# Kernel optimization log

Hardware: AMD Instinct MI355X
Metric: run time of the kernel (lower is better)

The kernel has to match this reference:

```python
import jax, jax.numpy as jnp
import numpy as np

K = 5            # self.k
MARGIN_CB = 0.05  # neighborhood_ranking_crossbrain default margin
MARGIN_NRC = 0.4  # self.margin used in partial_nrc_loss
MAX_PAIRS = 6
EPS = 1e-8


def _norm(x):
    return x / jnp.sqrt(jnp.sum(x * x, axis=-1, keepdims=True) + 1e-12)


def _cos_dist_pair(a, b):
    s = jnp.clip(jnp.sum(a * b, axis=-1), -1.0 + EPS, 1.0 - EPS)
    return 1.0 - s


def _pairwise_cos_dist(x, y):
    return 1.0 - _norm(x) @ _norm(y).T


def _sq_dist(x):
    # squared euclidean distance -- same argsort order as torch.cdist
    sq = jnp.sum(x * x, axis=-1)
    return jnp.maximum(sq[:, None] + sq[None, :] - 2.0 * (x @ x.T), 0.0)


def _crossbrain(z1, z2, key):
    # neighborhood_ranking_crossbrain with match_idx = identity (as in forward)
    N = z1.shape[0]
    D1 = jax.lax.stop_gradient(_sq_dist(z1))      # ranking only, no grad
    neigh = jnp.argsort(D1, axis=-1)[:, 1:K + 1]  # (N, K) nearest neighbors
    # sample K distinct negatives per token excluding {n} U neigh[n]:
    scores = jax.random.uniform(key, (N, N))
    rows = jnp.arange(N)
    scores = scores.at[rows[:, None], neigh].set(-jnp.inf)
    scores = scores.at[rows, rows].set(-jnp.inf)
    _, neg = jax.lax.top_k(scores, K)             # (N, K)
    z2n = _norm(z2)
    anchor = z2n[:, None, :]                      # (N,1,C)
    d_pos = _cos_dist_pair(anchor, z2n[neigh])    # (N, K)
    d_neg = _cos_dist_pair(anchor, z2n[neg])      # (N, K)
    return jnp.mean(jax.nn.relu(d_pos - d_neg + MARGIN_CB))


def _nrc_partial(A, B, key):
    # partial_matches_mnn + nrc_on_partial, fully vectorized & masked
    T = A.shape[0]
    D = jax.lax.stop_gradient(_pairwise_cos_dist(A, B))
    b_of_a = jnp.argmin(D, axis=1)
    a_of_b = jnp.argmin(D, axis=0)
    ar = jnp.arange(T)
    mutual = ar == a_of_b[b_of_a]                 # matched A tokens (injective)
    idxB_of_A = jnp.where(mutual, b_of_a, -1)
    is_matched_B = (jnp.zeros(T, jnp.int32).at[b_of_a].add(mutual.astype(jnp.int32)) > 0)
    DA = jax.lax.stop_gradient(_pairwise_cos_dist(A, A))
    neigh = jnp.argsort(DA, axis=-1)[:, 1:K + 1]  # (T, K)
    DB = _pairwise_cos_dist(B, B)                 # grads flow through DB
    posB = idxB_of_A[neigh]                       # (T, K)
    pos_mask = posB >= 0
    # negative pool: unmatched B tokens (stable argsort puts False first)
    order = jnp.argsort(is_matched_B)
    neg_count = jnp.maximum(T - jnp.sum(is_matched_B.astype(jnp.int32)), 1)
    r = jax.random.randint(key, (T, K), 0, T)
    negB = order[r % neg_count]                   # sample with replacement
    uB = jnp.maximum(idxB_of_A, 0)[:, None]
    d_pos = DB[uB, jnp.maximum(posB, 0)]
    d_neg = DB[uB, negB]
    hinge = jax.nn.relu(d_pos - d_neg + MARGIN_NRC) * pos_mask
    per_tok = jnp.sum(hinge, axis=1) / jnp.maximum(jnp.sum(pos_mask, axis=1), 1)
    valid = mutual & jnp.any(pos_mask, axis=1)
    cnt = jnp.sum(valid.astype(jnp.float32))
    return jnp.where(cnt > 0, jnp.sum(per_tok * valid) / jnp.maximum(cnt, 1.0), 0.0)


def _partial_nrc_loss(z1, z2, key, seed):
    Bn = z1.shape[0]
    pairs = [(p, q) for p in range(Bn) for q in range(Bn) if p != q]
    rng = np.random.RandomState(seed)
    if len(pairs) > MAX_PAIRS:
        sel = rng.permutation(len(pairs))[:MAX_PAIRS]
        pairs = [pairs[i] for i in sel]
    ps = jnp.array([p for p, _ in pairs])
    qs = jnp.array([q for _, q in pairs])
    keys = jax.random.split(key, len(pairs))
    losses = jax.vmap(_nrc_partial)(z1[ps], z2[qs], keys)
    return jnp.mean(losses)


def _taco_loss(z1, z2):
    Bn = z1.shape[0]
    base = jax.random.key(42)
    k1, k2, k3, k4 = jax.random.split(base, 4)
    loss2 = (jnp.sum(jax.vmap(_crossbrain)(z1, z2, jax.random.split(k1, Bn)))
             + jnp.sum(jax.vmap(_crossbrain)(z2, z1, jax.random.split(k2, Bn)))) / Bn
    loss3 = _partial_nrc_loss(z1, z2, k3, 0) + _partial_nrc_loss(z2, z1, k4, 1)
    return 10.0 * loss2 + 10.0 * loss3


def setup_inputs() -> dict:
    key = jax.random.key(0)
    k1, k2 = jax.random.split(key)
    Bn, T, C = 4, 2048, 768
    z1 = jax.random.normal(k1, (Bn, T, C), dtype=jnp.float32)
    z2 = jax.random.normal(k2, (Bn, T, C), dtype=jnp.float32)
    return {"z1": z1, "z2": z2}


def reference(z1, z2):
    return _taco_loss(z1, z2)
```

## Files before the change

kernel.cpp:

```cpp
#include <hip/hip_runtime.h>
#include <cstdint>
#include <cstddef>

#define TT 2048
#define CC 768
#define KK 5
#define PCAP 64

typedef __attribute__((ext_vector_type(8))) short short8;
typedef __attribute__((ext_vector_type(4))) short short4v;
typedef __attribute__((ext_vector_type(4))) float float4v;

struct PairTab { int sa[12]; int sb[12]; };
struct PairMap { int src[12]; int tr[12]; };

#define N_SELF_BLK (8 * 136)
#define TP 132

__device__ __forceinline__ unsigned int mix_hash(unsigned int a, unsigned int b) {
  unsigned long long x = (((unsigned long long)a) << 32) | (unsigned long long)b;
  x ^= x >> 33; x *= 0xff51afd7ed558ccdULL;
  x ^= x >> 33; x *= 0xc4ceb9fe1a85ec53ULL;
  x ^= x >> 33;
  return (unsigned int)(x & 0xffffffffu);
}

__device__ __forceinline__ unsigned short f2bf(float x) {
  union { float f; unsigned int u; } v; v.f = x;
  unsigned int r = v.u + 0x7fffu + ((v.u >> 16) & 1u);
  return (unsigned short)(r >> 16);
}

__device__ __forceinline__ float bf2f(unsigned short u) {
  union { unsigned int i; float f; } v; v.i = ((unsigned int)u) << 16; return v.f;
}

__device__ __forceinline__ void gload_lds16(const void* g, void* l) {
  __builtin_amdgcn_global_load_lds(
      (const __attribute__((address_space(1))) unsigned int*)g,
      (__attribute__((address_space(3))) unsigned int*)l, 16, 0, 0);
}

__device__ __forceinline__ bool lexlt(float k1, int i1, float k2, int i2) {
  return k1 < k2 || (k1 == k2 && i1 < i2);
}

#define INS5(kk_, ii_, L)                                                        \
  if (lexlt(kk_, ii_, L##k[4], L##i[4])) {                                       \
    L##k[4] = kk_; L##i[4] = ii_;                                                \
    if (lexlt(L##k[4], L##i[4], L##k[3], L##i[3])) {                             \
      float tk = L##k[3]; int ti_ = L##i[3]; L##k[3] = L##k[4]; L##i[3] = L##i[4]; L##k[4] = tk; L##i[4] = ti_; \
      if (lexlt(L##k[3], L##i[3], L##k[2], L##i[2])) {                           \
        tk = L##k[2]; ti_ = L##i[2]; L##k[2] = L##k[3]; L##i[2] = L##i[3]; L##k[3] = tk; L##i[3] = ti_; \
        if (lexlt(L##k[2], L##i[2], L##k[1], L##i[1])) {                         \
          tk = L##k[1]; ti_ = L##i[1]; L##k[1] = L##k[2]; L##i[1] = L##i[2]; L##k[2] = tk; L##i[2] = ti_; \
          if (lexlt(L##k[1], L##i[1], L##k[0], L##i[0])) {                       \
            tk = L##k[0]; ti_ = L##i[0]; L##k[0] = L##k[1]; L##i[0] = L##i[1]; L##k[1] = tk; L##i[1] = ti_; \
          }                                                                      \
        }                                                                        \
      }                                                                          \
    }                                                                            \
  }

__global__ __launch_bounds__(192) void prep_kernel(const float* __restrict__ z1, const float* __restrict__ z2,
                                                   unsigned short* __restrict__ zb, float* __restrict__ sq,
                                                   float* __restrict__ inv) {
  int r = blockIdx.x;
  const float* p = (r < 4 * TT) ? (z1 + (size_t)r * CC) : (z2 + (size_t)(r - 4 * TT) * CC);
  unsigned short* o = zb + (size_t)r * CC;
  float4 v = ((const float4*)p)[threadIdx.x];
  float s = v.x * v.x + v.y * v.y + v.z * v.z + v.w * v.w;
  ushort4 u;
  u.x = f2bf(v.x); u.y = f2bf(v.y); u.z = f2bf(v.z); u.w = f2bf(v.w);
  ((ushort4*)o)[threadIdx.x] = u;
#pragma unroll
  for (int off = 32; off > 0; off >>= 1) s += __shfl_down(s, off, 64);
  __shared__ float wred[3];
  int lane = threadIdx.x & 63, w = threadIdx.x >> 6;
  if (lane == 0) wred[w] = s;
  __syncthreads();
  if (threadIdx.x == 0) {
    float tot = wred[0] + wred[1] + wred[2];
    sq[r] = tot; inv[r] = rsqrtf(tot + 1e-12f);
  }
}

struct SmemKL { unsigned short As[128 * 64]; unsigned short Bs[128 * 64]; };
union SmemU {
  SmemKL st;
  unsigned short tile[128 * TP];
};

__device__ __forceinline__ void gram_mainloop(const unsigned short* __restrict__ A,
                                              const unsigned short* __restrict__ B,
                                              int bm, int bn, SmemKL& st, float4v (&acc)[4][4]) {
  const int lane = threadIdx.x & 63, waveId = threadIdx.x >> 6;
  const int wm = (waveId >> 1) * 64, wn = (waveId & 1) * 64;
  const int lrow = lane & 15, lquad = lane >> 4;
  for (int kk = 0; kk < CC; kk += 64) {
#pragma unroll
    for (int c = 0; c < 4; ++c) {
      int l = c * 256 + threadIdx.x;
      int row = l >> 3, pc = l & 7;
      int sc = pc ^ (row & 7);
      gload_lds16(A + (size_t)(bm + row) * CC + kk + sc * 8, &st.As[l * 8]);
      gload_lds16(B + (size_t)(bn + row) * CC + kk + sc * 8, &st.Bs[l * 8]);
    }
    __syncthreads();
#pragma unroll
    for (int h = 0; h < 2; ++h) {
      short8 af[4], bfr[4];
#pragma unroll
      for (int i = 0; i < 4; ++i) {
        int ra = wm + i * 16 + lrow;
        int ca = (h * 4 + lquad) ^ (ra & 7);
        af[i] = *(const short8*)&st.As[ra * 64 + ca * 8];
        int rb = wn + i * 16 + lrow;
        int cb2 = (h * 4 + lquad) ^ (rb & 7);
        bfr[i] = *(const short8*)&st.Bs[rb * 64 + cb2 * 8];
      }
#pragma unroll
      for (int i = 0; i < 4; ++i)
#pragma unroll
        for (int j = 0; j < 4; ++j)
          acc[i][j] = __builtin_amdgcn_mfma_f32_16x16x32_bf16(af[i], bfr[j], acc[i][j], 0, 0, 0);
    }
    __syncthreads();
  }
}

__global__ __launch_bounds__(256, 4) void gram_self(const unsigned short* __restrict__ zb,
                                                    unsigned short* __restrict__ gram) {
  __shared__ SmemU sm;
  const int bid = blockIdx.x;
  int s = bid / 136;
  int t = bid % 136;
  int ti = 0;
  while (t >= 16 - ti) { t -= 16 - ti; ++ti; }
  int tj = ti + t;
  int bm = ti * 128, bn = tj * 128;
  const unsigned short* A = zb + (size_t)s * TT * CC;

  float4v acc[4][4];
#pragma unroll
  for (int i = 0; i < 4; ++i)
#pragma unroll
    for (int j = 0; j < 4; ++j) acc[i][j] = (float4v){0.f, 0.f, 0.f, 0.f};

  gram_mainloop(A, A, bm, bn, sm.st, acc);

  const int lane = threadIdx.x & 63, waveId = threadIdx.x >> 6;
  const int wm = (waveId >> 1) * 64, wn = (waveId & 1) * 64;
  const int lrow = lane & 15, lquad = lane >> 4;

#pragma unroll
  for (int i = 0; i < 4; ++i)
#pragma unroll
    for (int j = 0; j < 4; ++j)
#pragma unroll
      for (int r = 0; r < 4; ++r) {
        int lr = wm + i * 16 + lquad * 4 + r;
        int lc = wn + j * 16 + lrow;
        sm.tile[lr * TP + lc] = f2bf(acc[i][j][r]);
      }
  __syncthreads();
  unsigned short* G = gram + (size_t)s * TT * TT;
  for (int it = 0; it < 16; ++it) {
    int task = it * 256 + threadIdx.x;
    int r = task >> 5;
    int c = task & 31;
    short4v v = *(const short4v*)&sm.tile[r * TP + c * 4];
    *(short4v*)&G[(size_t)(bm + r) * TT + bn + c * 4] = v;
  }
  if (bm != bn) {
    for (int it = 0; it < 16; ++it) {
      int task = it * 256 + threadIdx.x;
      int cc = task >> 5;
      int q = task & 31;
      short4v v;
      v[0] = (short)sm.tile[(q * 4 + 0) * TP + cc];
      v[1] = (short)sm.tile[(q * 4 + 1) * TP + cc];
      v[2] = (short)sm.tile[(q * 4 + 2) * TP + cc];
      v[3] = (short)sm.tile[(q * 4 + 3) * TP + cc];
      *(short4v*)&G[(size_t)(bn + cc) * TT + bm + q * 4] = v;
    }
  }
}

__global__ __launch_bounds__(256, 4) void gram_cross(const unsigned short* __restrict__ zb,
                                                     const float* __restrict__ invAll, PairTab tab,
                                                     float* __restrict__ prow_v, int* __restrict__ prow_i,
                                                     float* __restrict__ pcol_v, int* __restrict__ pcol_i) {
  __shared__ SmemKL smk;
  __shared__ float sInvA[128], sInvB[128];
  __shared__ float rowv[2][128]; __shared__ int rowi[2][128];
  __shared__ float colv[2][128]; __shared__ int coli[2][128];

  const int cbid = blockIdx.x;
  const int p = cbid >> 8;
  const int tile = cbid & 255;
  const int bn = (tile & 15) * 128;
  const int bm = (tile >> 4) * 128;
  const unsigned short* A = zb + (size_t)tab.sa[p] * TT * CC;
  const unsigned short* B = zb + (size_t)tab.sb[p] * TT * CC;
  if (threadIdx.x < 128) sInvA[threadIdx.x] = invAll[(size_t)tab.sa[p] * TT + bm + threadIdx.x];
  else sInvB[threadIdx.x - 128] = invAll[(size_t)tab.sb[p] * TT + bn + threadIdx.x - 128];

  float4v acc[4][4];
#pragma unroll
  for (int i = 0; i < 4; ++i)
#pragma unroll
    for (int j = 0; j < 4; ++j) acc[i][j] = (float4v){0.f, 0.f, 0.f, 0.f};

  gram_mainloop(A, B, bm, bn, smk, acc);

  const int lane = threadIdx.x & 63, waveId = threadIdx.x >> 6;
  const int wm = (waveId >> 1) * 64, wn = (waveId & 1) * 64;
  const int lrow = lane & 15, lquad = lane >> 4;

  float rbv[4][4]; int rbi[4][4];
#pragma unroll
  for (int i = 0; i < 4; ++i)
#pragma unroll
    for (int r = 0; r < 4; ++r) { rbv[i][r] = INFINITY; rbi[i][r] = TT; }
#pragma unroll
  for (int i = 0; i < 4; ++i)
#pragma unroll
    for (int j = 0; j < 4; ++j) {
      int col = bn + wn + j * 16 + lrow;
      float ivb = sInvB[wn + j * 16 + lrow];
#pragma unroll
      for (int r = 0; r < 4; ++r) {
        float v = -acc[i][j][r] * ivb;
        if (v < rbv[i][r]) { rbv[i][r] = v; rbi[i][r] = col; }
      }
    }
#pragma unroll
  for (int m = 1; m <= 8; m <<= 1) {
#pragma unroll
    for (int i = 0; i < 4; ++i)
#pragma unroll
      for (int r = 0; r < 4; ++r) {
        float v2 = __shfl_xor(rbv[i][r], m, 64);
        int i2 = __shfl_xor(rbi[i][r], m, 64);
        if (v2 < rbv[i][r] || (v2 == rbv[i][r] && i2 < rbi[i][r])) { rbv[i][r] = v2; rbi[i][r] = i2; }
      }
  }
  if (lrow == 0) {
#pragma unroll
    for (int i = 0; i < 4; ++i)
#pragma unroll
      for (int r = 0; r < 4; ++r) {
        int lr = wm + i * 16 + lquad * 4 + r;
        rowv[wn >> 6][lr] = rbv[i][r]; rowi[wn >> 6][lr] = rbi[i][r];
      }
  }

  float cbv[4]; int cbi[4];
#pragma unroll
  for (int j = 0; j < 4; ++j) { cbv[j] = INFINITY; cbi[j] = TT; }
#pragma unroll
  for (int j = 0; j < 4; ++j)
#pragma unroll
    for (int i = 0; i < 4; ++i)
#pragma unroll
      for (int r = 0; r < 4; ++r) {
        int lr = wm + i * 16 + lquad * 4 + r;
        float v = -acc[i][j][r] * sInvA[lr];
        if (v < cbv[j]) { cbv[j] = v; cbi[j] = bm + lr; }
      }
#pragma unroll
  for (int m = 16; m <= 32; m <<= 1) {
#pragma unroll
    for (int j = 0; j < 4; ++j) {
      float v2 = __shfl_xor(cbv[j], m, 64);
      int i2 = __shfl_xor(cbi[j], m, 64);
      if (v2 < cbv[j] || (v2 == cbv[j] && i2 < cbi[j])) { cbv[j] = v2; cbi[j] = i2; }
    }
  }
  if (lquad == 0) {
#pragma unroll
    for (int j = 0; j < 4; ++j) {
      int lc = wn + j * 16 + lrow;
      colv[wm >> 6][lc] = cbv[j]; coli[wm >> 6][lc] = cbi[j];
    }
  }
  __syncthreads();

  int bj = bn >> 7, bi2 = bm >> 7;
  if (threadIdx.x < 128) {
    int t = threadIdx.x;
    float v0 = rowv[0][t], v1 = rowv[1][t];
    int i0 = rowi[0][t], i1 = rowi[1][t];
    bool take1 = (v1 < v0) || (v1 == v0 && i1 < i0);
    prow_v[((size_t)p * 16 + bj) * TT + bm + t] = take1 ? v1 : v0;
    prow_i[((size_t)p * 16 + bj) * TT + bm + t] = take1 ? i1 : i0;
  } else {
    int t = threadIdx.x - 128;
    float v0 = colv[0][t], v1 = colv[1][t];
    int i0 = coli[0][t], i1 = coli[1][t];
    bool take1 = (v1 < v0) || (v1 == v0 && i1 < i0);
    pcol_v[((size_t)p * 16 + bi2) * TT + bn + t] = take1 ? v1 : v0;
    pcol_i[((size_t)p * 16 + bi2) * TT + bn + t] = take1 ? i1 : i0;
  }
}

__device__ void top5_row_full(const unsigned short* __restrict__ G, const float* __restrict__ sq,
                              const float* __restrict__ inv, int i, int lane,
                              int* __restrict__ o0, int* __restrict__ o1) {
  float ak[5]; int ai[5];
  float bk[5]; int bi[5];
#pragma unroll
  for (int t = 0; t < 5; ++t) { ak[t] = INFINITY; ai[t] = TT; bk[t] = INFINITY; bi[t] = TT; }
#pragma unroll
  for (int step = 0; step < 8; ++step) {
    int j4 = (step * 64 + lane) * 4;
    ushort4 g4u = *(const ushort4*)&G[j4];
    float4 s4 = *(const float4*)&sq[j4];
    float4 v4 = *(const float4*)&inv[j4];
#pragma unroll
    for (int c = 0; c < 4; ++c) {
      int j = j4 + c;
      float g = bf2f((c == 0) ? g4u.x : (c == 1) ? g4u.y : (c == 2) ? g4u.z : g4u.w);
      float sv = (c == 0) ? s4.x : (c == 1) ? s4.y : (c == 2) ? s4.z : s4.w;
      float iv = (c == 0) ? v4.x : (c == 1) ? v4.y : (c == 2) ? v4.z : v4.w;
      float k0 = (j == i) ? INFINITY : sv - 2.f * g;
      float k1 = (j == i) ? INFINITY : -g * iv;
      INS5(k0, j, a)
      INS5(k1, j, b)
    }
  }
#pragma unroll
  for (int m = 1; m <= 32; m <<= 1) {
    float ok[5]; int oi[5];
#pragma unroll
    for (int t = 0; t < 5; ++t) { ok[t] = __shfl_xor(ak[t], m, 64); oi[t] = __shfl_xor(ai[t], m, 64); }
#pragma unroll
    for (int t = 0; t < 5; ++t) { INS5(ok[t], oi[t], a) }
#pragma unroll
    for (int t = 0; t < 5; ++t) { ok[t] = __shfl_xor(bk[t], m, 64); oi[t] = __shfl_xor(bi[t], m, 64); }
#pragma unroll
    for (int t = 0; t < 5; ++t) { INS5(ok[t], oi[t], b) }
  }
  if (lane < KK) {
    int v0 = (lane == 0) ? ai[0] : (lane == 1) ? ai[1] : (lane == 2) ? ai[2] : (lane == 3) ? ai[3] : ai[4];
    int v1 = (lane == 0) ? bi[0] : (lane == 1) ? bi[1] : (lane == 2) ? bi[2] : (lane == 3) ? bi[3] : bi[4];
    o0[lane] = v0;
    o1[lane] = v1;
  }
}

__device__ void top5_body(int s, int bx, const unsigned short* __restrict__ gram,
                          const float* __restrict__ sqAll, const float* __restrict__ invAll,
                          int* __restrict__ out0, int* __restrict__ out1) {
  int w = threadIdx.x >> 6, lane = threadIdx.x & 63;
  int i = bx * 4 + w;
  const unsigned short* G = gram + (size_t)s * TT * TT + (size_t)i * TT;
  const float* sq = sqAll + (size_t)s * TT;
  const float* inv = invAll + (size_t)s * TT;

  __shared__ ushort4 rowc4[4][TT / 4];
  __shared__ float pvv[4][2][PCAP];
  __shared__ int pix[4][2][PCAP];
  __shared__ int pcnt[4][2];
  if (lane < 2) pcnt[w][lane] = 0;

  float mn0 = INFINITY, mn1 = INFINITY;
#pragma unroll
  for (int step = 0; step < 8; ++step) {
    int jc = step * 64 + lane;
    int j4 = jc * 4;
    ushort4 g4u = *(const ushort4*)&G[j4];
    rowc4[w][jc] = g4u;
    float4 s4 = *(const float4*)&sq[j4];
    float4 v4 = *(const float4*)&inv[j4];
#pragma unroll
    for (int c = 0; c < 4; ++c) {
      int j = j4 + c;
      float g = bf2f((c == 0) ? g4u.x : (c == 1) ? g4u.y : (c == 2) ? g4u.z : g4u.w);
      float sv = (c == 0) ? s4.x : (c == 1) ? s4.y : (c == 2) ? s4.z : s4.w;
      float iv = (c == 0) ? v4.x : (c == 1) ? v4.y : (c == 2) ? v4.z : v4.w;
      float k0 = (j == i) ? INFINITY : sv - 2.f * g;
      float k1 = (j == i) ? INFINITY : -g * iv;
      mn0 = fminf(mn0, k0);
      mn1 = fminf(mn1, k1);
    }
  }
#pragma unroll
  for (int m = 1; m <= 4; m <<= 1) {
    mn0 = fminf(mn0, __shfl_xor(mn0, m, 64));
    mn1 = fminf(mn1, __shfl_xor(mn1, m, 64));
  }
  float gv0[8], gv1[8];
#pragma unroll
  for (int g = 0; g < 8; ++g) {
    gv0[g] = __shfl(mn0, g * 8, 64);
    gv1[g] = __shfl(mn1, g * 8, 64);
  }
  float T0 = 0.f, T1 = 0.f;
#pragma unroll
  for (int g = 0; g < 8; ++g) {
    int r0 = 0, r1 = 0;
#pragma unroll
    for (int h = 0; h < 8; ++h) {
      r0 += ((gv0[h] < gv0[g]) || (gv0[h] == gv0[g] && h < g)) ? 1 : 0;
      r1 += ((gv1[h] < gv1[g]) || (gv1[h] == gv1[g] && h < g)) ? 1 : 0;
    }
    if (r0 == 4) T0 = gv0[g];
    if (r1 == 4) T1 = gv1[g];
  }

#pragma unroll
  for (int step = 0; step < 8; ++step) {
    int jc = step * 64 + lane;
    int j4 = jc * 4;
    ushort4 g4u = rowc4[w][jc];
    float4 s4 = *(const float4*)&sq[j4];
    float4 v4 = *(const float4*)&inv[j4];
#pragma unroll
    for (int c = 0; c < 4; ++c) {
      int j = j4 + c;
      float g = bf2f((c == 0) ? g4u.x : (c == 1) ? g4u.y : (c == 2) ? g4u.z : g4u.w);
      float sv = (c == 0) ? s4.x : (c == 1) ? s4.y : (c == 2) ? s4.z : s4.w;
      float iv = (c == 0) ? v4.x : (c == 1) ? v4.y : (c == 2) ? v4.z : v4.w;
      float k0 = (j == i) ? INFINITY : sv - 2.f * g;
      float k1 = (j == i) ? INFINITY : -g * iv;
      bool c0 = (k0 <= T0), c1 = (k1 <= T1);
      if (__any(c0)) {
        if (c0) {
          int q = atomicAdd(&pcnt[w][0], 1);
          if (q < PCAP) { pvv[w][0][q] = k0; pix[w][0][q] = j; }
        }
      }
      if (__any(c1)) {
        if (c1) {
          int q = atomicAdd(&pcnt[w][1], 1);
          if (q < PCAP) { pvv[w][1][q] = k1; pix[w][1][q] = j; }
        }
      }
    }
  }

  int c0n = pcnt[w][0], c1n = pcnt[w][1];
  if (c0n > PCAP || c1n > PCAP) {
    top5_row_full(G, sq, inv, i, lane,
                  out0 + ((size_t)s * TT + i) * KK, out1 + ((size_t)s * TT + i) * KK);
    return;
  }
  {
    float cv = (lane < c0n) ? pvv[w][0][lane] : INFINITY;
    int ci = (lane < c0n) ? pix[w][0][lane] : TT;
    int r = 0;
    for (int t = 0; t < c0n; ++t) {
      float ov = pvv[w][0][t]; int oi = pix[w][0][t];
      r += lexlt(ov, oi, cv, ci) ? 1 : 0;
    }
    if (lane < c0n && r < KK) out0[((size_t)s * TT + i) * KK + r] = ci;
  }
  {
    float cv = (lane < c1n) ? pvv[w][1][lane] : INFINITY;
    int ci = (lane < c1n) ? pix[w][1][lane] : TT;
    int r = 0;
    for (int t = 0; t < c1n; ++t) {
      float ov = pvv[w][1][t]; int oi = pix[w][1][t];
      r += lexlt(ov, oi, cv, ci) ? 1 : 0;
    }
    if (lane < c1n && r < KK) out1[((size_t)s * TT + i) * KK + r] = ci;
  }
}

__device__ void argmin_body(int bx, int p, const float* __restrict__ prow_v, const int* __restrict__ prow_i,
                            const float* __restrict__ pcol_v, const int* __restrict__ pcol_i,
                            const PairMap& pm,
                            int* __restrict__ b_of_a, int* __restrict__ a_of_b) {
  int u = pm.src[p];
  bool tr = pm.tr[p] != 0;
  int t = bx * 256 + threadIdx.x;
  int isRow = t < TT;
  int x = isRow ? t : t - TT;
  bool useRow = (isRow != 0) != tr;
  const float* pv = (useRow ? prow_v : pcol_v) + (size_t)u * 16 * TT;
  const int* pi = (useRow ? prow_i : pcol_i) + (size_t)u * 16 * TT;
  float best = INFINITY; int bidx = TT;
  for (int s = 0; s < 16; ++s) {
    float v = pv[(size_t)s * TT + x]; int id = pi[(size_t)s * TT + x];
    if (v < best || (v == best && id < bidx)) { best = v; bidx = id; }
  }
  if (isRow) b_of_a[(size_t)p * TT + x] = bidx;
  else       a_of_b[(size_t)p * TT + x] = bidx;
}

__global__ __launch_bounds__(256) void top5_argmin_fused(const unsigned short* __restrict__ gram,
                                                         const float* __restrict__ sqAll,
                                                         const float* __restrict__ invAll,
                                                         int* __restrict__ out0, int* __restrict__ out1,
                                                         const float* __restrict__ prow_v, const int* __restrict__ prow_i,
                                                         const float* __restrict__ pcol_v, const int* __restrict__ pcol_i,
                                                         PairMap pm,
                                                         int* __restrict__ b_of_a, int* __restrict__ a_of_b) {
  unsigned int b = blockIdx.x;
  if (b < 4096) {
    top5_body((int)(b >> 9), (int)(b & 511), gram, sqAll, invAll, out0, out1);
  } else {
    unsigned int t = b - 4096;
    argmin_body((int)(t & 15), (int)(t >> 4), prow_v, prow_i, pcol_v, pcol_i, pm, b_of_a, a_of_b);
  }
}

__device__ void cb_hinge_body(int bx, int c, const unsigned short* __restrict__ gram, const float* __restrict__ invAll,
                              const int* __restrict__ neigh1, float* __restrict__ cb_acc) {
  int i0 = bx * 64;
  int sa = c, sb = (c < 4) ? (c + 4) : (c - 4);
  const unsigned short* Gs = gram + (size_t)sb * TT * TT;
  const float* invB = invAll + (size_t)sb * TT;
  const int* neighA = neigh1 + (size_t)sa * TT * KK;
  unsigned int seed = 0x13579BDFu + 0x9E3779B9u * (unsigned)c;
  int tid = threadIdx.x;

  __shared__ int targ[64][10];
  __shared__ float sval[64][10];
  for (int t = tid; t < 64 * KK; t += 256) targ[t / KK][t % KK] = neighA[(size_t)i0 * KK + t];
  __syncthreads();
  if (tid < 64) {
    int i = i0 + tid;
    int pos[KK];
#pragma unroll
    for (int k = 0; k < KK; ++k) pos[k] = targ[tid][k];
    unsigned int ctr = 0;
    for (int k = 0; k < KK; ++k) {
      int cand;
      while (true) {
        unsigned int h = mix_hash(seed ^ (unsigned)i, ctr++);
        cand = (int)(h & (TT - 1));
        bool bad = (cand == i);
        for (int t = 0; t < KK; ++t) bad = bad || (cand == pos[t]);
        for (int t = 0; t < k; ++t) bad = bad || (cand == targ[tid][KK + t]);
        if (!bad) break;
      }
      targ[tid][KK + k] = cand;
    }
  }
  __syncthreads();
  for (int t = tid; t < 640; t += 256) {
    int il = t / 10, k = t % 10;
    int tt = targ[il][k];
    sval[il][k] = bf2f(Gs[(size_t)(i0 + il) * TT + tt]) * invB[tt];
  }
  __syncthreads();
  if (tid < 64) {
    int i = i0 + tid;
    float ii = invB[i];
    const float lo = -1.f + 1e-8f, hi = 1.f - 1e-8f;
    float hsum = 0.f;
#pragma unroll
    for (int k = 0; k < KK; ++k) {
      float sp = fminf(fmaxf(sval[tid][k] * ii, lo), hi);
      float sn = fminf(fmaxf(sval[tid][KK + k] * ii, lo), hi);
      float h = sn - sp + 0.05f;
      hsum += (h > 0.f) ? h : 0.f;
    }
#pragma unroll
    for (int off = 32; off > 0; off >>= 1) hsum += __shfl_down(hsum, off, 64);
    if (tid == 0) atomicAdd(&cb_acc[c], hsum);
  }
}

__device__ void mutual_body(int p, const int* __restrict__ b_of_a_all,
                            const int* __restrict__ a_of_b_all,
                            int* __restrict__ idxB_all, int* __restrict__ matchedB_all,
                            int* __restrict__ unmatched_all, int* __restrict__ scalars_all) {
  const int* b_of_a = b_of_a_all + (size_t)p * TT;
  const int* a_of_b = a_of_b_all + (size_t)p * TT;
  int* idxB_of_A = idxB_all + (size_t)p * TT;
  int* matchedB = matchedB_all + (size_t)p * TT;
  int* unmatched = unmatched_all + (size_t)p * TT;
  __shared__ int cnt_sh;
  for (int j = threadIdx.x; j < TT; j += 256) matchedB[j] = 0;
  __syncthreads();
  for (int i = threadIdx.x; i < TT; i += 256) {
    int b = b_of_a[i];
    bool mut = (a_of_b[b] == i);
    idxB_of_A[i] = mut ? b : -1;
    if (mut) matchedB[b] = 1;
  }
  __syncthreads();
  if (threadIdx.x == 0) cnt_sh = 0;
  __syncthreads();
  for (int j = threadIdx.x; j < TT; j += 256) {
    if (!matchedB[j]) { int q = atomicAdd(&cnt_sh, 1); unmatched[q] = j; }
  }
  __syncthreads();
  if (threadIdx.x == 0) {
    int c = cnt_sh;
    if (c == 0) { unmatched[0] = 0; c = 1; }
    scalars_all[p * 16] = c;
  }
}

__global__ __launch_bounds__(256) void cb_mutual_fused(const unsigned short* __restrict__ gram,
                                                       const float* __restrict__ invAll,
                                                       const int* __restrict__ neigh1, float* __restrict__ cb_acc,
                                                       const int* __restrict__ b_of_a, const int* __restrict__ a_of_b,
                                                       int* __restrict__ idxB_all, int* __restrict__ matchedB_all,
                                                       int* __restrict__ unmatched_all, int* __restrict__ scalars_all) {
  unsigned int b = blockIdx.x;
  if (b < 256) {
    cb_hinge_body((int)(b & 31), (int)(b >> 5), gram, invAll, neigh1, cb_acc);
  } else {
    mutual_body((int)(b - 256), b_of_a, a_of_b, idxB_all, matchedB_all, unmatched_all, scalars_all);
  }
}

__global__ __launch_bounds__(256) void nrc_hinge_block(const unsigned short* __restrict__ gram, const float* __restrict__ invAll,
                                                       const int* __restrict__ neighC, const int* __restrict__ idxB_all,
                                                       const int* __restrict__ unmatched_all,
                                                       const int* __restrict__ scalars_all,
                                                       PairTab tab, float* __restrict__ nrc_acc) {
  int p = blockIdx.y;
  int i0 = blockIdx.x * 64;
  int sa = tab.sa[p], sb = tab.sb[p];
  const unsigned short* Gs = gram + (size_t)sb * TT * TT;
  const float* invB = invAll + (size_t)sb * TT;
  const int* neighA = neighC + (size_t)sa * TT * KK;
  const int* idxB_of_A = idxB_all + (size_t)p * TT;
  const int* unmatched = unmatched_all + (size_t)p * TT;
  unsigned int seed = 0xC0FFEE11u + 0x9E3779B9u * (unsigned)p;
  float* acc = nrc_acc + p * 2;
  int tid = threadIdx.x;

  __shared__ int targ[64][10];
  __shared__ float sval[64][10];
  __shared__ unsigned int tmask[64];
  __shared__ int su[64];
  if (tid < 64) { tmask[tid] = 0; su[tid] = idxB_of_A[i0 + tid]; }
  __syncthreads();
  unsigned int neg_count = (unsigned int)scalars_all[p * 16];
  for (int t = tid; t < 64 * KK; t += 256) {
    int il = t / KK, k = t % KK;
    int nb = neighA[(size_t)i0 * KK + t];
    int pb = idxB_of_A[nb];
    targ[il][k] = (pb >= 0) ? pb : 0;
    if (pb >= 0) atomicOr(&tmask[il], 1u << k);
  }
  for (int t = tid; t < 64 * KK; t += 256) {
    int il = t / KK, k = t % KK;
    int i = i0 + il;
    unsigned int r = mix_hash(seed ^ 0xA5A5u, (unsigned)(i * KK + k)) & (TT - 1);
    targ[il][KK + k] = unmatched[r % neg_count];
  }
  __syncthreads();
  for (int t = tid; t < 640; t += 256) {
    int il = t / 10, k = t % 10;
    int u = su[il] >= 0 ? su[il] : 0;
    int tt = targ[il][k];
    sval[il][k] = bf2f(Gs[(size_t)u * TT + tt]) * invB[tt];
  }
  __syncthreads();
  if (tid < 64) {
    int idx = su[tid];
    int u = idx >= 0 ? idx : 0;
    float iu = invB[u];
    unsigned int tm = tmask[tid];
    float hsum = 0.f; int pcnt = 0;
#pragma unroll
    for (int k = 0; k < KK; ++k) {
      if (tm & (1u << k)) {
        float dpos = 1.f - sval[tid][k] * iu;
        float dneg = 1.f - sval[tid][KK + k] * iu;
        float h = dpos - dneg + 0.4f;
        hsum += (h > 0.f) ? h : 0.f;
        pcnt++;
      }
    }
    float hs = 0.f, vc = 0.f;
    if (idx >= 0 && pcnt > 0) { hs = hsum / (float)pcnt; vc = 1.0f; }
#pragma unroll
    for (int off = 32; off > 0; off >>= 1) {
      hs += __shfl_down(hs, off, 64);
      vc += __shfl_down(vc, off, 64);
    }
    if (tid == 0) {
      atomicAdd(&acc[0], hs);
      atomicAdd(&acc[1], vc);
    }
  }
}

__global__ void final_kernel(const float* __restrict__ cb_acc, const float* __restrict__ nrc_acc,
                             float* __restrict__ out) {
  float loss2 = 0.f;
  for (int c = 0; c < 8; ++c) loss2 += cb_acc[c] * (1.0f / 10240.0f);
  loss2 *= 0.25f;
  float loss3 = 0.f;
  for (int d = 0; d < 2; ++d) {
    float s = 0.f;
    for (int t = 0; t < 6; ++t) {
      float cnt = nrc_acc[(d * 6 + t) * 2 + 1];
      float sum = nrc_acc[(d * 6 + t) * 2 + 0];
      s += (cnt > 0.f) ? (sum / cnt) : 0.f;
    }
    loss3 += s * (1.f / 6.f);
  }
  out[0] = 10.f * loss2 + 10.f * loss3;
}

namespace {
struct MT19937 {
  uint32_t mt[624]; int mti;
  void seed(uint32_t s) {
    mt[0] = s;
    for (int i = 1; i < 624; ++i) mt[i] = 1812433253u * (mt[i - 1] ^ (mt[i - 1] >> 30)) + (uint32_t)i;
    mti = 624;
  }
  uint32_t next() {
    if (mti >= 624) {
      for (int i = 0; i < 624; ++i) {
        uint32_t y = (mt[i] & 0x80000000u) | (mt[(i + 1) % 624] & 0x7fffffffu);
        uint32_t v = y >> 1;
        if (y & 1u) v ^= 0x9908b0dfu;
        mt[i] = mt[(i + 397) % 624] ^ v;
      }
      mti = 0;
    }
    uint32_t y = mt[mti++];
    y ^= y >> 11; y ^= (y << 7) & 0x9d2c5680u; y ^= (y << 15) & 0xefc60000u; y ^= y >> 18;
    return y;
  }
  uint32_t interval(uint32_t mx) {
    uint32_t mask = mx;
    mask |= mask >> 1; mask |= mask >> 2; mask |= mask >> 4; mask |= mask >> 8; mask |= mask >> 16;
    while (true) { uint32_t v = next() & mask; if (v <= mx) return v; }
  }
};
inline void np_perm12_first6(uint32_t seed, int* sel6) {
  int a[12]; for (int i = 0; i < 12; ++i) a[i] = i;
  MT19937 r; r.seed(seed);
  for (int i = 11; i >= 1; --i) { uint32_t j = r.interval((uint32_t)i); int t = a[i]; a[i] = a[j]; a[j] = t; }
  for (int i = 0; i < 6; ++i) sel6[i] = a[i];
}
}

extern "C" void kernel_launch(void* const* d_in, const int* in_sizes, int n_in,
                              void* d_out, int out_size, void* d_ws, size_t ws_size,
                              hipStream_t stream) {
  const float* z1 = (const float*)d_in[0];
  const float* z2 = (const float*)d_in[1];
  float* out = (float*)d_out;

  char* base = (char*)d_ws;
  size_t off = 0;
  auto alloc = [&](size_t bytes) -> void* {
    void* p = base + off;
    off = (off + bytes + 255) & ~(size_t)255;
    return p;
  };
  unsigned short* gram   = (unsigned short*)alloc((size_t)8 * TT * TT * 2);
  unsigned short* zb     = (unsigned short*)alloc((size_t)8 * TT * CC * 2);
  float* sq              = (float*)alloc((size_t)8 * TT * 4);
  float* inv             = (float*)alloc((size_t)8 * TT * 4);
  int*   neigh1          = (int*)alloc((size_t)8 * TT * KK * 4);
  int*   neighC          = (int*)alloc((size_t)8 * TT * KK * 4);
  float* prow_v          = (float*)alloc((size_t)12 * 16 * TT * 4);
  int*   prow_i          = (int*)alloc((size_t)12 * 16 * TT * 4);
  float* pcol_v          = (float*)alloc((size_t)12 * 16 * TT * 4);
  int*   pcol_i          = (int*)alloc((size_t)12 * 16 * TT * 4);
  int*   b_of_a          = (int*)alloc((size_t)12 * TT * 4);
  int*   a_of_b          = (int*)alloc((size_t)12 * TT * 4);
  int*   idxB            = (int*)alloc((size_t)12 * TT * 4);
  int*   matchedB        = (int*)alloc((size_t)12 * TT * 4);
  int*   unmatched       = (int*)alloc((size_t)12 * TT * 4);
  int*   scalars         = (int*)alloc(12 * 16 * 4);
  float* accs            = (float*)alloc(64 * 4);
  float* cb_acc          = accs;
  float* nrc_acc         = accs + 8;

  hipMemsetAsync(accs, 0, 64 * 4, stream);

  int sel0[6], sel1[6];
  np_perm12_first6(0u, sel0);
  np_perm12_first6(1u, sel1);
  static const int PP[12] = {0, 0, 0, 1, 1, 1, 2, 2, 2, 3, 3, 3};
  static const int QQ[12] = {1, 2, 3, 0, 2, 3, 0, 1, 3, 0, 1, 2};
  PairTab tab;
  for (int d = 0; d < 2; ++d) {
    const int* sel = (d == 0) ? sel0 : sel1;
    for (int t = 0; t < 6; ++t) {
      int pi_ = PP[sel[t]], qi = QQ[sel[t]];
      int p = d * 6 + t;
      tab.sa[p] = (d == 0) ? pi_ : 4 + pi_;
      tab.sb[p] = (d == 0) ? 4 + qi : qi;
    }
  }

  PairTab gtab; PairMap pm; int nU = 0;
  for (int p = 0; p < 12; ++p) {
    int f = -1, ftr = 0;
    for (int q = 0; q < nU; ++q) {
      if (gtab.sa[q] == tab.sb[p] && gtab.sb[q] == tab.sa[p]) { f = q; ftr = 1; break; }
      if (gtab.sa[q] == tab.sa[p] && gtab.sb[q] == tab.sb[p]) { f = q; ftr = 0; break; }
    }
    if (f >= 0) { pm.src[p] = f; pm.tr[p] = ftr; }
    else { gtab.sa[nU] = tab.sa[p]; gtab.sb[nU] = tab.sb[p]; pm.src[p] = nU; pm.tr[p] = 0; ++nU; }
  }

  prep_kernel<<<8 * TT, 192, 0, stream>>>(z1, z2, zb, sq, inv);

  gram_self<<<N_SELF_BLK, 256, 0, stream>>>(zb, gram);

  gram_cross<<<nU * 256, 256, 0, stream>>>(zb, inv, gtab, prow_v, prow_i, pcol_v, pcol_i);

  top5_argmin_fused<<<4096 + 192, 256, 0, stream>>>(gram, sq, inv, neigh1, neighC,
                                                    prow_v, prow_i, pcol_v, pcol_i, pm, b_of_a, a_of_b);

  cb_mutual_fused<<<256 + 12, 256, 0, stream>>>(gram, inv, neigh1, cb_acc,
                                                b_of_a, a_of_b, idxB, matchedB, unmatched, scalars);

  nrc_hinge_block<<<dim3(TT / 64, 12), 256, 0, stream>>>(gram, inv, neighC, idxB, unmatched, scalars, tab, nrc_acc);

  final_kernel<<<1, 1, 0, stream>>>(cb_acc, nrc_acc, out);
}
```

Before: 300.7 us.

## Fuse per-tile row minima into gram_self epilogue and enlarge gram_cross tiles

The gram_self epilogue now computes per-128-column-tile minima of the squared-distance and cosine keys for each row, and for the transposed block. top5 then derives its pruning threshold from these 16 partial minima instead of scanning the row twice and caching it in shared memory. gram_cross moves to 256x128 tiles with its own inline main loop, halving the block count and reusing B tiles more, at the cost of occupancy (launch bounds drop to 2). The accumulator memset is folded into prep_kernel, and top5 gets an extra fallback when fewer than K candidates survive.

```diff
diff --git a/kernel.cpp b/kernel.cpp
--- a/kernel.cpp
+++ b/kernel.cpp
@@ -64,8 +64,9 @@
 
 __global__ __launch_bounds__(192) void prep_kernel(const float* __restrict__ z1, const float* __restrict__ z2,
                                                    unsigned short* __restrict__ zb, float* __restrict__ sq,
-                                                   float* __restrict__ inv) {
+                                                   float* __restrict__ inv, float* __restrict__ accs) {
   int r = blockIdx.x;
+  if (r == 0 && threadIdx.x < 64) accs[threadIdx.x] = 0.f;
   const float* p = (r < 4 * TT) ? (z1 + (size_t)r * CC) : (z2 + (size_t)(r - 4 * TT) * CC);
   unsigned short* o = zb + (size_t)r * CC;
   float4 v = ((const float4*)p)[threadIdx.x];
@@ -130,8 +131,12 @@
 }
 
 __global__ __launch_bounds__(256, 4) void gram_self(const unsigned short* __restrict__ zb,
-                                                    unsigned short* __restrict__ gram) {
+                                                    unsigned short* __restrict__ gram,
+                                                    const float* __restrict__ sqAll,
+                                                    const float* __restrict__ invAll,
+                                                    float* __restrict__ pmin0, float* __restrict__ pmin1) {
   __shared__ SmemU sm;
+  __shared__ float sqN[128], invN[128], sqM[128], invM[128];
   const int bid = blockIdx.x;
   int s = bid / 136;
   int t = bid % 136;
@@ -140,6 +145,10 @@
   int tj = ti + t;
   int bm = ti * 128, bn = tj * 128;
   const unsigned short* A = zb + (size_t)s * TT * CC;
+  const float* sqS = sqAll + (size_t)s * TT;
+  const float* invS = invAll + (size_t)s * TT;
+  if (threadIdx.x < 128) { sqN[threadIdx.x] = sqS[bn + threadIdx.x]; invN[threadIdx.x] = invS[bn + threadIdx.x]; }
+  else { sqM[threadIdx.x - 128] = sqS[bm + threadIdx.x - 128]; invM[threadIdx.x - 128] = invS[bm + threadIdx.x - 128]; }
 
   float4v acc[4][4];
 #pragma unroll
@@ -185,50 +194,115 @@
       *(short4v*)&G[(size_t)(bn + cc) * TT + bm + q * 4] = v;
     }
   }
-}
-
-__global__ __launch_bounds__(256, 4) void gram_cross(const unsigned short* __restrict__ zb,
+  if (threadIdx.x < 128) {
+    int r = threadIdx.x;
+    float m0 = INFINITY, m1 = INFINITY;
+    for (int c = 0; c < 128; ++c) {
+      if (bm == bn && c == r) continue;
+      float g = bf2f(sm.tile[r * TP + c]);
+      m0 = fminf(m0, sqN[c] - 2.f * g);
+      m1 = fminf(m1, -g * invN[c]);
+    }
+    pmin0[((size_t)s * 16 + (bn >> 7)) * TT + bm + r] = m0;
+    pmin1[((size_t)s * 16 + (bn >> 7)) * TT + bm + r] = m1;
+  } else if (bm != bn) {
+    int c = threadIdx.x - 128;
+    float m0 = INFINITY, m1 = INFINITY;
+    for (int r = 0; r < 128; ++r) {
+      float g = bf2f(sm.tile[r * TP + c]);
+      m0 = fminf(m0, sqM[r] - 2.f * g);
+      m1 = fminf(m1, -g * invM[r]);
+    }
+    pmin0[((size_t)s * 16 + (bm >> 7)) * TT + bn + c] = m0;
+    pmin1[((size_t)s * 16 + (bm >> 7)) * TT + bn + c] = m1;
+  }
+}
+
+__global__ __launch_bounds__(256, 2) void gram_cross(const unsigned short* __restrict__ zb,
                                                      const float* __restrict__ invAll, PairTab tab,
                                                      float* __restrict__ prow_v, int* __restrict__ prow_i,
                                                      float* __restrict__ pcol_v, int* __restrict__ pcol_i) {
-  __shared__ SmemKL smk;
-  __shared__ float sInvA[128], sInvB[128];
-  __shared__ float rowv[2][128]; __shared__ int rowi[2][128];
-  __shared__ float colv[2][128]; __shared__ int coli[2][128];
+  __shared__ union {
+    struct { unsigned short As[256 * 64]; unsigned short Bs[128 * 64]; } st;
+    struct { float rowv[2][256]; int rowi[2][256]; float colv[2][128]; int coli[2][128]; } ep;
+  } sm;
+  __shared__ float sInvA[256], sInvB[128];
 
   const int cbid = blockIdx.x;
-  const int p = cbid >> 8;
-  const int tile = cbid & 255;
+  const int p = cbid >> 7;
+  const int tile = cbid & 127;
   const int bn = (tile & 15) * 128;
-  const int bm = (tile >> 4) * 128;
+  const int bm = (tile >> 4) * 256;
   const unsigned short* A = zb + (size_t)tab.sa[p] * TT * CC;
   const unsigned short* B = zb + (size_t)tab.sb[p] * TT * CC;
-  if (threadIdx.x < 128) sInvA[threadIdx.x] = invAll[(size_t)tab.sa[p] * TT + bm + threadIdx.x];
-  else sInvB[threadIdx.x - 128] = invAll[(size_t)tab.sb[p] * TT + bn + threadIdx.x - 128];
-
-  float4v acc[4][4];
-#pragma unroll
-  for (int i = 0; i < 4; ++i)
+  sInvA[threadIdx.x] = invAll[(size_t)tab.sa[p] * TT + bm + threadIdx.x];
+  if (threadIdx.x < 128) sInvB[threadIdx.x] = invAll[(size_t)tab.sb[p] * TT + bn + threadIdx.x];
+
+  const int lane = threadIdx.x & 63, waveId = threadIdx.x >> 6;
+  const int wr = waveId >> 1, wc = waveId & 1;
+  const int lrow = lane & 15, lquad = lane >> 4;
+
+  float4v acc[8][4];
+#pragma unroll
+  for (int i = 0; i < 8; ++i)
 #pragma unroll
     for (int j = 0; j < 4; ++j) acc[i][j] = (float4v){0.f, 0.f, 0.f, 0.f};
 
-  gram_mainloop(A, B, bm, bn, smk, acc);
-
-  const int lane = threadIdx.x & 63, waveId = threadIdx.x >> 6;
-  const int wm = (waveId >> 1) * 64, wn = (waveId & 1) * 64;
-  const int lrow = lane & 15, lquad = lane >> 4;
-
-  float rbv[4][4]; int rbi[4][4];
-#pragma unroll
-  for (int i = 0; i < 4; ++i)
+  for (int kk = 0; kk < CC; kk += 64) {
+#pragma unroll
+    for (int c = 0; c < 8; ++c) {
+      int l = c * 256 + threadIdx.x;
+      int row = l >> 3, pc = l & 7;
+      int sc = pc ^ (row & 7);
+      gload_lds16(A + (size_t)(bm + row) * CC + kk + sc * 8, &sm.st.As[l * 8]);
+    }
+#pragma unroll
+    for (int c = 0; c < 4; ++c) {
+      int l = c * 256 + threadIdx.x;
+      int row = l >> 3, pc = l & 7;
+      int sc = pc ^ (row & 7);
+      gload_lds16(B + (size_t)(bn + row) * CC + kk + sc * 8, &sm.st.Bs[l * 8]);
+    }
+    __syncthreads();
+#pragma unroll
+    for (int h = 0; h < 2; ++h) {
+      short8 bfr[4];
+#pragma unroll
+      for (int j = 0; j < 4; ++j) {
+        int rb = wc * 64 + j * 16 + lrow;
+        int cb2 = (h * 4 + lquad) ^ (rb & 7);
+        bfr[j] = *(const short8*)&sm.st.Bs[rb * 64 + cb2 * 8];
+      }
+#pragma unroll
+      for (int ih = 0; ih < 2; ++ih) {
+        short8 af[4];
+#pragma unroll
+        for (int i2 = 0; i2 < 4; ++i2) {
+          int ra = wr * 128 + (ih * 4 + i2) * 16 + lrow;
+          int ca = (h * 4 + lquad) ^ (ra & 7);
+          af[i2] = *(const short8*)&sm.st.As[ra * 64 + ca * 8];
+        }
+#pragma unroll
+        for (int i2 = 0; i2 < 4; ++i2)
+#pragma unroll
+          for (int j = 0; j < 4; ++j)
+            acc[ih * 4 + i2][j] = __builtin_amdgcn_mfma_f32_16x16x32_bf16(af[i2], bfr[j], acc[ih * 4 + i2][j], 0, 0, 0);
+      }
+    }
+    __syncthreads();
+  }
+
+  float rbv[8][4]; int rbi[8][4];
+#pragma unroll
+  for (int i = 0; i < 8; ++i)
 #pragma unroll
     for (int r = 0; r < 4; ++r) { rbv[i][r] = INFINITY; rbi[i][r] = TT; }
 #pragma unroll
-  for (int i = 0; i < 4; ++i)
+  for (int i = 0; i < 8; ++i)
 #pragma unroll
     for (int j = 0; j < 4; ++j) {
-      int col = bn + wn + j * 16 + lrow;
-      float ivb = sInvB[wn + j * 16 + lrow];
+      int col = bn + wc * 64 + j * 16 + lrow;
+      float ivb = sInvB[wc * 64 + j * 16 + lrow];
 #pragma unroll
       for (int r = 0; r < 4; ++r) {
         float v = -acc[i][j][r] * ivb;
@@ -238,7 +312,7 @@
 #pragma unroll
   for (int m = 1; m <= 8; m <<= 1) {
 #pragma unroll
-    for (int i = 0; i < 4; ++i)
+    for (int i = 0; i < 8; ++i)
 #pragma unroll
       for (int r = 0; r < 4; ++r) {
         float v2 = __shfl_xor(rbv[i][r], m, 64);
@@ -248,11 +322,11 @@
   }
   if (lrow == 0) {
 #pragma unroll
-    for (int i = 0; i < 4; ++i)
+    for (int i = 0; i < 8; ++i)
 #pragma unroll
       for (int r = 0; r < 4; ++r) {
-        int lr = wm + i * 16 + lquad * 4 + r;
-        rowv[wn >> 6][lr] = rbv[i][r]; rowi[wn >> 6][lr] = rbi[i][r];
+        int lr = wr * 128 + i * 16 + lquad * 4 + r;
+        sm.ep.rowv[wc][lr] = rbv[i][r]; sm.ep.rowi[wc][lr] = rbi[i][r];
       }
   }
 
@@ -262,10 +336,10 @@
 #pragma unroll
   for (int j = 0; j < 4; ++j)
 #pragma unroll
-    for (int i = 0; i < 4; ++i)
+    for (int i = 0; i < 8; ++i)
 #pragma unroll
       for (int r = 0; r < 4; ++r) {
-        int lr = wm + i * 16 + lquad * 4 + r;
+        int lr = wr * 128 + i * 16 + lquad * 4 + r;
         float v = -acc[i][j][r] * sInvA[lr];
         if (v < cbv[j]) { cbv[j] = v; cbi[j] = bm + lr; }
       }
@@ -281,27 +355,26 @@
   if (lquad == 0) {
 #pragma unroll
     for (int j = 0; j < 4; ++j) {
-      int lc = wn + j * 16 + lrow;
-      colv[wm >> 6][lc] = cbv[j]; coli[wm >> 6][lc] = cbi[j];
-    }
-  }
-  __syncthreads();
-
-  int bj = bn >> 7, bi2 = bm >> 7;
-  if (threadIdx.x < 128) {
+      int lc = wc * 64 + j * 16 + lrow;
+      sm.ep.colv[wr][lc] = cbv[j]; sm.ep.coli[wr][lc] = cbi[j];
+    }
+  }
+  __syncthreads();
+
+  int bj = bn >> 7;
+  {
     int t = threadIdx.x;
-    float v0 = rowv[0][t], v1 = rowv[1][t];
-    int i0 = rowi[0][t], i1 = rowi[1][t];
+    float v0 = sm.ep.rowv[0][t], v1 = sm.ep.rowv[1][t];
+    int i0 = sm.ep.rowi[0][t], i1 = sm.ep.rowi[1][t];
     bool take1 = (v1 < v0) || (v1 == v0 && i1 < i0);
     prow_v[((size_t)p * 16 + bj) * TT + bm + t] = take1 ? v1 : v0;
     prow_i[((size_t)p * 16 + bj) * TT + bm + t] = take1 ? i1 : i0;
-  } else {
-    int t = threadIdx.x - 128;
-    float v0 = colv[0][t], v1 = colv[1][t];
-    int i0 = coli[0][t], i1 = coli[1][t];
-    bool take1 = (v1 < v0) || (v1 == v0 && i1 < i0);
-    pcol_v[((size_t)p * 16 + bi2) * TT + bn + t] = take1 ? v1 : v0;
-    pcol_i[((size_t)p * 16 + bi2) * TT + bn + t] = take1 ? i1 : i0;
+  }
+  {
+    int wrh = threadIdx.x >> 7, c = threadIdx.x & 127;
+    int slab = (bm >> 7) + wrh;
+    pcol_v[((size_t)p * 16 + slab) * TT + bn + c] = sm.ep.colv[wrh][c];
+    pcol_i[((size_t)p * 16 + slab) * TT + bn + c] = sm.ep.coli[wrh][c];
   }
 }
 
@@ -352,6 +425,7 @@
 
 __device__ void top5_body(int s, int bx, const unsigned short* __restrict__ gram,
                           const float* __restrict__ sqAll, const float* __restrict__ invAll,
+                          const float* __restrict__ pmin0, const float* __restrict__ pmin1,
                           int* __restrict__ out0, int* __restrict__ out1) {
   int w = threadIdx.x >> 6, lane = threadIdx.x & 63;
   int i = bx * 4 + w;
@@ -359,62 +433,33 @@
   const float* sq = sqAll + (size_t)s * TT;
   const float* inv = invAll + (size_t)s * TT;
 
-  __shared__ ushort4 rowc4[4][TT / 4];
   __shared__ float pvv[4][2][PCAP];
   __shared__ int pix[4][2][PCAP];
   __shared__ int pcnt[4][2];
   if (lane < 2) pcnt[w][lane] = 0;
 
-  float mn0 = INFINITY, mn1 = INFINITY;
+  int t16 = lane & 15;
+  float m0 = pmin0[((size_t)s * 16 + t16) * TT + i];
+  float m1 = pmin1[((size_t)s * 16 + t16) * TT + i];
+  int r0 = 0, r1 = 0;
+#pragma unroll
+  for (int d = 1; d < 16; ++d) {
+    int h = (t16 + d) & 15;
+    int src = (lane & 48) | h;
+    float o0 = __shfl(m0, src, 64);
+    float o1 = __shfl(m1, src, 64);
+    r0 += (o0 < m0 || (o0 == m0 && h < t16)) ? 1 : 0;
+    r1 += (o1 < m1 || (o1 == m1 && h < t16)) ? 1 : 0;
+  }
+  unsigned long long b0 = __ballot(r0 == 4);
+  unsigned long long b1 = __ballot(r1 == 4);
+  float T0 = __shfl(m0, (int)(__ffsll(b0) - 1), 64);
+  float T1 = __shfl(m1, (int)(__ffsll(b1) - 1), 64);
+
 #pragma unroll
   for (int step = 0; step < 8; ++step) {
-    int jc = step * 64 + lane;
-    int j4 = jc * 4;
+    int j4 = (step * 64 + lane) * 4;
     ushort4 g4u = *(const ushort4*)&G[j4];
-    rowc4[w][jc] = g4u;
-    float4 s4 = *(const float4*)&sq[j4];
-    float4 v4 = *(const float4*)&inv[j4];
-#pragma unroll
-    for (int c = 0; c < 4; ++c) {
-      int j = j4 + c;
-      float g = bf2f((c == 0) ? g4u.x : (c == 1) ? g4u.y : (c == 2) ? g4u.z : g4u.w);
-      float sv = (c == 0) ? s4.x : (c == 1) ? s4.y : (c == 2) ? s4.z : s4.w;
-      float iv = (c == 0) ? v4.x : (c == 1) ? v4.y : (c == 2) ? v4.z : v4.w;
-      float k0 = (j == i) ? INFINITY : sv - 2.f * g;
-      float k1 = (j == i) ? INFINITY : -g * iv;
-      mn0 = fminf(mn0, k0);
-      mn1 = fminf(mn1, k1);
-    }
-  }
-#pragma unroll
-  for (int m = 1; m <= 4; m <<= 1) {
-    mn0 = fminf(mn0, __shfl_xor(mn0, m, 64));
-    mn1 = fminf(mn1, __shfl_xor(mn1, m, 64));
-  }
-  float gv0[8], gv1[8];
-#pragma unroll
-  for (int g = 0; g < 8; ++g) {
-    gv0[g] = __shfl(mn0, g * 8, 64);
-    gv1[g] = __shfl(mn1, g * 8, 64);
-  }
-  float T0 = 0.f, T1 = 0.f;
-#pragma unroll
-  for (int g = 0; g < 8; ++g) {
-    int r0 = 0, r1 = 0;
-#pragma unroll
-    for (int h = 0; h < 8; ++h) {
-      r0 += ((gv0[h] < gv0[g]) || (gv0[h] == gv0[g] && h < g)) ? 1 : 0;
-      r1 += ((gv1[h] < gv1[g]) || (gv1[h] == gv1[g] && h < g)) ? 1 : 0;
-    }
-    if (r0 == 4) T0 = gv0[g];
-    if (r1 == 4) T1 = gv1[g];
-  }
-
-#pragma unroll
-  for (int step = 0; step < 8; ++step) {
-    int jc = step * 64 + lane;
-    int j4 = jc * 4;
-    ushort4 g4u = rowc4[w][jc];
     float4 s4 = *(const float4*)&sq[j4];
     float4 v4 = *(const float4*)&inv[j4];
 #pragma unroll
@@ -442,7 +487,7 @@
   }
 
   int c0n = pcnt[w][0], c1n = pcnt[w][1];
-  if (c0n > PCAP || c1n > PCAP) {
+  if (c0n > PCAP || c1n > PCAP || c0n < KK || c1n < KK) {
     top5_row_full(G, sq, inv, i, lane,
                   out0 + ((size_t)s * TT + i) * KK, out1 + ((size_t)s * TT + i) * KK);
     return;
@@ -493,6 +538,8 @@
 __global__ __launch_bounds__(256) void top5_argmin_fused(const unsigned short* __restrict__ gram,
                                                          const float* __restrict__ sqAll,
                                                          const float* __restrict__ invAll,
+                                                         const float* __restrict__ pmin0,
+                                                         const float* __restrict__ pmin1,
                                                          int* __restrict__ out0, int* __restrict__ out1,
                                                          const float* __restrict__ prow_v, const int* __restrict__ prow_i,
                                                          const float* __restrict__ pcol_v, const int* __restrict__ pcol_i,
@@ -500,7 +547,7 @@
                                                          int* __restrict__ b_of_a, int* __restrict__ a_of_b) {
   unsigned int b = blockIdx.x;
   if (b < 4096) {
-    top5_body((int)(b >> 9), (int)(b & 511), gram, sqAll, invAll, out0, out1);
+    top5_body((int)(b >> 9), (int)(b & 511), gram, sqAll, invAll, pmin0, pmin1, out0, out1);
   } else {
     unsigned int t = b - 4096;
     argmin_body((int)(t & 15), (int)(t >> 4), prow_v, prow_i, pcol_v, pcol_i, pm, b_of_a, a_of_b);
@@ -760,6 +807,8 @@
   float* inv             = (float*)alloc((size_t)8 * TT * 4);
   int*   neigh1          = (int*)alloc((size_t)8 * TT * KK * 4);
   int*   neighC          = (int*)alloc((size_t)8 * TT * KK * 4);
+  float* pmin0           = (float*)alloc((size_t)8 * 16 * TT * 4);
+  float* pmin1           = (float*)alloc((size_t)8 * 16 * TT * 4);
   float* prow_v          = (float*)alloc((size_t)12 * 16 * TT * 4);
   int*   prow_i          = (int*)alloc((size_t)12 * 16 * TT * 4);
   float* pcol_v          = (float*)alloc((size_t)12 * 16 * TT * 4);
@@ -774,8 +823,6 @@
   float* cb_acc          = accs;
   float* nrc_acc         = accs + 8;
 
-  hipMemsetAsync(accs, 0, 64 * 4, stream);
-
   int sel0[6], sel1[6];
   np_perm12_first6(0u, sel0);
   np_perm12_first6(1u, sel1);
@@ -803,13 +850,13 @@
     else { gtab.sa[nU] = tab.sa[p]; gtab.sb[nU] = tab.sb[p]; pm.src[p] = nU; pm.tr[p] = 0; ++nU; }
   }
 
-  prep_kernel<<<8 * TT, 192, 0, stream>>>(z1, z2, zb, sq, inv);
-
-  gram_self<<<N_SELF_BLK, 256, 0, stream>>>(zb, gram);
-
-  gram_cross<<<nU * 256, 256, 0, stream>>>(zb, inv, gtab, prow_v, prow_i, pcol_v, pcol_i);
-
-  top5_argmin_fused<<<4096 + 192, 256, 0, stream>>>(gram, sq, inv, neigh1, neighC,
+  prep_kernel<<<8 * TT, 192, 0, stream>>>(z1, z2, zb, sq, inv, accs);
+
+  gram_self<<<N_SELF_BLK, 256, 0, stream>>>(zb, gram, sq, inv, pmin0, pmin1);
+
+  gram_cross<<<nU * 128, 256, 0, stream>>>(zb, inv, gtab, prow_v, prow_i, pcol_v, pcol_i);
+
+  top5_argmin_fused<<<4096 + 192, 256, 0, stream>>>(gram, sq, inv, pmin0, pmin1, neigh1, neighC,
                                                     prow_v, prow_i, pcol_v, pcol_i, pm, b_of_a, a_of_b);
 
   cb_mutual_fused<<<256 + 12, 256, 0, stream>>>(gram, inv, neigh1, cb_acc,
```

After: 379.7 us. 1.26x slower.
